# Optimization experiments

Hardware: AMD Instinct MI355X
Metric: run time of the kernel (lower is better)

Reference implementation:

```python
import jax, jax.numpy as jnp
import numpy as np

N_BRANCH, N_LAYER = 4, 3
B, T, D_IN = 4, 1024, 32
D_MODEL, D_INNER, D_STATE, D_CONV, DT_RANK = 128, 256, 16, 4, 8
EMBED = 64
MAX_NORM = 10.0  # safe_expmap0 tangent-norm clip
EPS = 1e-7


def setup_inputs() -> dict:
    key = jax.random.key(0)
    ks = jax.random.split(key, 12)
    def nrm(k, shp, s=0.02):
        return s * jax.random.normal(k, shp, dtype=jnp.float32)
    A_init = jnp.log(jnp.arange(1, D_STATE + 1, dtype=jnp.float32))
    return {
        "trend": jax.random.normal(ks[0], (B, T, D_IN), jnp.float32),
        "seasonal_coarse": jax.random.normal(ks[1], (B, T, D_IN), jnp.float32),
        "seasonal_fine": jax.random.normal(ks[2], (B, T, D_IN), jnp.float32),
        "residual": jax.random.normal(ks[3], (B, T, D_IN), jnp.float32),
        "W_ip": nrm(ks[4], (N_BRANCH, D_IN, D_MODEL)),
        "b_ip": jnp.zeros((N_BRANCH, D_MODEL), jnp.float32),
        "W_in": nrm(ks[5], (N_BRANCH, N_LAYER, D_MODEL, 2 * D_INNER)),
        "conv_w": nrm(ks[6], (N_BRANCH, N_LAYER, D_INNER, D_CONV), 0.1),
        "conv_b": jnp.zeros((N_BRANCH, N_LAYER, D_INNER), jnp.float32),
        "W_x": nrm(ks[7], (N_BRANCH, N_LAYER, D_INNER, DT_RANK + 2 * D_STATE)),
        "W_dt": nrm(ks[8], (N_BRANCH, N_LAYER, DT_RANK, D_INNER), 0.1),
        "b_dt": jnp.full((N_BRANCH, N_LAYER, D_INNER), -4.6, jnp.float32),  # softplus ~ 0.01
        "A_log": jnp.broadcast_to(A_init, (N_BRANCH, N_LAYER, D_INNER, D_STATE)),
        "D_param": jnp.ones((N_BRANCH, N_LAYER, D_INNER), jnp.float32),
        "W_out": nrm(ks[9], (N_BRANCH, N_LAYER, D_INNER, D_MODEL)),
        "W_op": nrm(ks[10], (N_BRANCH, D_MODEL, EMBED)),
        "b_op": jnp.zeros((N_BRANCH, EMBED), jnp.float32),
        "eff_scale": jnp.asarray(0.1, jnp.float32),
    }


def _mamba_layer(x, Win, cw, cb, Wx, Wdt, bdt, Alog, Dp, Wout):
    # x: [B, T, d_model]
    Tlen = x.shape[1]
    xz = x @ Win                                   # [B,T,2*di]
    xp, z = jnp.split(xz, 2, axis=-1)
    # causal depthwise conv1d, kernel D_CONV
    xpad = jnp.pad(xp, ((0, 0), (D_CONV - 1, 0), (0, 0)))
    xc = sum(xpad[:, k:k + Tlen, :] * cw[:, k] for k in range(D_CONV))
    xc = jax.nn.silu(xc + cb)                      # [B,T,di]
    dbl = xc @ Wx                                  # [B,T,r+2s]
    dt = jax.nn.softplus(dbl[..., :DT_RANK] @ Wdt + bdt)   # [B,T,di]
    Bm = dbl[..., DT_RANK:DT_RANK + D_STATE]       # [B,T,s]
    Cm = dbl[..., DT_RANK + D_STATE:]              # [B,T,s]
    A = -jnp.exp(Alog)                             # [di,s]
    dA = jnp.exp(dt[..., None] * A)                # [B,T,di,s]
    dBx = (dt * xc)[..., None] * Bm[:, :, None, :] # [B,T,di,s]

    def step(h, inp):
        dA_t, dBx_t, C_t = inp
        h = dA_t * h + dBx_t
        return h, jnp.einsum('bds,bs->bd', h, C_t)

    h0 = jnp.zeros((x.shape[0], D_INNER, D_STATE), x.dtype)
    _, ys = jax.lax.scan(step, h0, (jnp.swapaxes(dA, 0, 1),
                                     jnp.swapaxes(dBx, 0, 1),
                                     jnp.swapaxes(Cm, 0, 1)))
    y = jnp.swapaxes(ys, 0, 1) + Dp * xc
    return (y * jax.nn.silu(z)) @ Wout


def _embed(x, Wip, bip, Wins, cws, cbs, Wxs, Wdts, bdts, Alogs, Dps, Wouts, Wop, bop):
    h = x @ Wip + bip
    for l in range(N_LAYER):
        h = _mamba_layer(h, Wins[l], cws[l], cbs[l], Wxs[l], Wdts[l], bdts[l],
                         Alogs[l], Dps[l], Wouts[l])
    return h.mean(axis=1) @ Wop + bop              # [B, EMBED]


def _expmap0(v):
    # safe expmap0 on Lorentz (k=1): clip tangent norm at MAX_NORM
    n = jnp.linalg.norm(v, axis=-1, keepdims=True)
    nc = jnp.clip(n, EPS, MAX_NORM)
    v = v * (nc / jnp.maximum(n, EPS))
    return jnp.concatenate([jnp.cosh(nc), jnp.sinh(nc) / nc * v], axis=-1)


def _projx(x):
    sp = x[..., 1:]
    t = jnp.sqrt(1.0 + jnp.sum(sp * sp, axis=-1, keepdims=True))
    return jnp.concatenate([t, sp], axis=-1)


def _logmap0(x):
    sp = x[..., 1:]
    t = jnp.maximum(x[..., :1], 1.0 + EPS)
    d = jnp.arccosh(t)
    spn = jnp.maximum(jnp.linalg.norm(sp, axis=-1, keepdims=True), EPS)
    return d * sp / spn


def _forward(trend, seasonal_coarse, seasonal_fine, residual,
             W_ip, b_ip, W_in, conv_w, conv_b, W_x, W_dt, b_dt,
             A_log, D_param, W_out, W_op, b_op, eff_scale):
    xs = [trend, seasonal_coarse, seasonal_fine, residual]
    z_t = [
        _embed(xs[b], W_ip[b], b_ip[b], W_in[b], conv_w[b], conv_b[b], W_x[b],
               W_dt[b], b_dt[b], A_log[b], D_param[b], W_out[b], W_op[b], b_op[b])
        for b in range(N_BRANCH)
    ]
    es = jnp.tanh(eff_scale)
    z_h = [_projx(_expmap0(z * es)) for z in z_t]
    us = [_logmap0(zh) for zh in z_h]
    combined_tangent = us[0] + us[1] + us[2] + us[3]
    combined_h = _projx(_expmap0(combined_tangent * es))
    return (*z_t, *z_h, combined_tangent, combined_h)


def reference(trend, seasonal_coarse, seasonal_fine, residual,
              W_ip, b_ip, W_in, conv_w, conv_b, W_x, W_dt, b_dt,
              A_log, D_param, W_out, W_op, b_op, eff_scale):
    return _forward(trend, seasonal_coarse, seasonal_fine, residual,
                    W_ip, b_ip, W_in, conv_w, conv_b, W_x, W_dt, b_dt,
                    A_log, D_param, W_out, W_op, b_op, eff_scale)
```

## Files before the change

### kernel.cpp

```cpp
#include <hip/hip_runtime.h>
#include <math.h>

#define NBR 4
#define NLAY 3
#define Bk 4
#define Tk 1024
#define DIN 32
#define DMODEL 128
#define DINNER 256
#define DSTATE 16
#define DTRANK 8
#define EMBEDk 64
#define BT (Bk*Tk)
#define EPSF 1e-7f
#define MAXNF 10.0f
#define LCH 64
#define NCH (Tk/LCH)
#define UF 8
#define NWB 320

typedef __bf16 bf16x8 __attribute__((ext_vector_type(8)));
typedef float  f32x4  __attribute__((ext_vector_type(4)));
typedef unsigned short u16x8 __attribute__((ext_vector_type(8)));
typedef unsigned short u16x4 __attribute__((ext_vector_type(4)));

__device__ __forceinline__ float siluf(float x){ return x / (1.f + __expf(-x)); }
__device__ __forceinline__ float softplusf(float x){ return (x > 20.f) ? x : log1pf(__expf(x)); }
__device__ __forceinline__ unsigned short f2b(float x){
    union { float f; unsigned u; } v; v.f = x;
    unsigned r = v.u + 0x7FFF + ((v.u >> 16) & 1);
    return (unsigned short)(r >> 16);
}
__device__ __forceinline__ float b2f(unsigned short u){
    union { unsigned u; float f; } v; v.u = ((unsigned)u) << 16; return v.f;
}

__device__ __forceinline__ void gll16(const void* g, void* l){
    __builtin_amdgcn_global_load_lds(
        (const __attribute__((address_space(1))) unsigned int*)g,
        (__attribute__((address_space(3))) unsigned int*)l,
        16, 0, 0);
}

__device__ __forceinline__ void dA_pow8(float q, int sh, float* dA){
    const float q2 = q * q, q4 = q2 * q2, q8 = q4 * q4;
    const float f = sh ? q8 : 1.0f;
    dA[0] = q * f;       dA[1] = q2 * f;
    dA[2] = q2 * q * f;  dA[3] = q4 * f;
    dA[4] = q4 * q * f;  dA[5] = q4 * q2 * f;
    dA[6] = q4 * q2 * q * f; dA[7] = q8 * f;
}

template<int MODE>
__global__ __launch_bounds__(256) void bgemm_k(
    const unsigned short* __restrict__ Ab, long aBr, int K,
    const unsigned short* __restrict__ Bt, long bBr,
    unsigned short* __restrict__ Cu0, long cu0Br,
    unsigned short* __restrict__ Cu1, long cu1Br,
    float* __restrict__ Cf, long cfBr,
    const float* __restrict__ bias, long biasBr)
{
    const int br = blockIdx.z;
    Ab += (long)br * aBr;
    Bt += (long)br * bBr;
    Cu0 += (long)br * cu0Br;
    if (MODE == 0) Cu1 += (long)br * cu1Br;
    if (MODE == 3) { Cf += (long)br * cfBr; bias += (long)br * biasBr; }
    const int m0 = blockIdx.x * 64, n0 = blockIdx.y * 64;
    __shared__ __align__(16) unsigned short As[8 * 64 * 8];
    __shared__ __align__(16) unsigned short Bs[8 * 64 * 8];
    const int tid = threadIdx.x;
    const int lane = tid & 63, w = tid >> 6;
    const int wm = w >> 1, wn = w & 1;
    const int quad = lane >> 4, l15 = lane & 15;
    f32x4 acc00 = {0,0,0,0}, acc01 = {0,0,0,0}, acc10 = {0,0,0,0}, acc11 = {0,0,0,0};
    for (int kc = 0; kc < K; kc += 64) {
        #pragma unroll
        for (int it = 0; it < 2; ++it) {
            const int kch = w + it * 4;
            gll16(Ab + (long)(m0 + lane) * K + kc + kch * 8, &As[(kch * 64) * 8]);
            gll16(Bt + (long)(n0 + lane) * K + kc + kch * 8, &Bs[(kch * 64) * 8]);
        }
        __syncthreads();
        #pragma unroll
        for (int k0 = 0; k0 < 64; k0 += 32) {
            const int kch = (k0 >> 3) + quad;
            bf16x8 a0 = *(const bf16x8*)&As[(kch * 64 + wm * 32 +      l15) * 8];
            bf16x8 a1 = *(const bf16x8*)&As[(kch * 64 + wm * 32 + 16 + l15) * 8];
            bf16x8 b0 = *(const bf16x8*)&Bs[(kch * 64 + wn * 32 +      l15) * 8];
            bf16x8 b1 = *(const bf16x8*)&Bs[(kch * 64 + wn * 32 + 16 + l15) * 8];
            acc00 = __builtin_amdgcn_mfma_f32_16x16x32_bf16(a0, b0, acc00, 0, 0, 0);
            acc01 = __builtin_amdgcn_mfma_f32_16x16x32_bf16(a0, b1, acc01, 0, 0, 0);
            acc10 = __builtin_amdgcn_mfma_f32_16x16x32_bf16(a1, b0, acc10, 0, 0, 0);
            acc11 = __builtin_amdgcn_mfma_f32_16x16x32_bf16(a1, b1, acc11, 0, 0, 0);
        }
        __syncthreads();
    }
    #pragma unroll
    for (int e = 0; e < 4; ++e) {
        f32x4 a = (e == 0) ? acc00 : (e == 1) ? acc01 : (e == 2) ? acc10 : acc11;
        const int msub = (e >> 1) * 16, nsub = (e & 1) * 16;
        const int col = n0 + wn * 32 + nsub + l15;
        #pragma unroll
        for (int r = 0; r < 4; ++r) {
            const int row = m0 + wm * 32 + msub + quad * 4 + r;
            const float v = a[r];
            if (MODE == 0) {
                if (n0 < 256) Cu0[(long)row * 256 + col] = f2b(v);
                else          Cu1[(long)row * 256 + (col - 256)] = f2b(siluf(v));
            } else {
                if (col < 256)      Cu0[(long)row * 256 + col] = f2b(softplusf(v + bias[col]));
                else if (col < 288) Cf[(long)row * 32 + (col - 256)] = v;
            }
        }
    }
}

__global__ __launch_bounds__(256) void sgemmWT_k(
    const float* __restrict__ Wout, const float* __restrict__ Win,
    const float* __restrict__ Wip, const float* __restrict__ bip,
    const float* __restrict__ Wop,
    unsigned short* __restrict__ WfT, float* __restrict__ Weq,
    float* __restrict__ Wcomb)
{
    const int z = blockIdx.z;
    const int tid = threadIdx.x;
    const int tx = tid & 15, ty = tid >> 4;
    __shared__ float As_[32][68];
    __shared__ float Bs_[32][68];
    float acc[4][4] = {};
    if (z < 8) {
        const int p = z >> 2, br = z & 3;
        const float* A  = Wout + (long)(br * NLAY + p) * DINNER * DMODEL;
        const float* Bw = Win  + (long)(br * NLAY + p + 1) * DMODEL * 512;
        const int m0 = blockIdx.x * 64, n0 = blockIdx.y * 64;
        for (int kc = 0; kc < DMODEL; kc += 32) {
            #pragma unroll
            for (int it = 0; it < 2; ++it) {
                int id = tid + it * 256;
                int r = id >> 3, c4 = (id & 7) << 2;
                float4 v = *(const float4*)(A + (long)(m0 + r) * DMODEL + kc + c4);
                As_[c4+0][r] = v.x; As_[c4+1][r] = v.y; As_[c4+2][r] = v.z; As_[c4+3][r] = v.w;
                int rb = id >> 4, cb = (id & 15) << 2;
                *(float4*)&Bs_[rb][cb] = *(const float4*)(Bw + (long)(kc + rb) * 512 + n0 + cb);
            }
            __syncthreads();
            #pragma unroll
            for (int kk = 0; kk < 32; ++kk) {
                float4 a4 = *(const float4*)&As_[kk][ty << 2];
                float4 b4 = *(const float4*)&Bs_[kk][tx << 2];
                float av[4] = {a4.x, a4.y, a4.z, a4.w};
                float bv[4] = {b4.x, b4.y, b4.z, b4.w};
                #pragma unroll
                for (int i = 0; i < 4; ++i)
                    #pragma unroll
                    for (int j = 0; j < 4; ++j)
                        acc[i][j] = fmaf(av[i], bv[j], acc[i][j]);
            }
            __syncthreads();
        }
        unsigned short* o = WfT + (long)z * 512 * 256;
        const int row0 = m0 + (ty << 2), col = n0 + (tx << 2);
        #pragma unroll
        for (int j = 0; j < 4; ++j) {
            u16x4 v;
            #pragma unroll
            for (int i = 0; i < 4; ++i) v[i] = f2b(acc[i][j]);
            *(u16x4*)(o + (long)(col + j) * 256 + row0) = v;
        }
    } else if (z == 8) {
        const int br = blockIdx.x;
        const float* A  = Wip + (long)br * DIN * DMODEL;
        const float* bp = bip + (long)br * DMODEL;
        const float* Bw = Win + (long)br * NLAY * DMODEL * 512;
        const int n0 = blockIdx.y * 64;
        for (int kc = 0; kc < DMODEL; kc += 32) {
            #pragma unroll
            for (int it = 0; it < 2; ++it) {
                int id = tid + it * 256;
                int r = id >> 3, c4 = (id & 7) << 2;
                float4 v;
                if (r < 32)       v = *(const float4*)(A + (long)r * DMODEL + kc + c4);
                else if (r == 32) v = *(const float4*)(bp + kc + c4);
                else              { v.x = 0.f; v.y = 0.f; v.z = 0.f; v.w = 0.f; }
                As_[c4+0][r] = v.x; As_[c4+1][r] = v.y; As_[c4+2][r] = v.z; As_[c4+3][r] = v.w;
                int rb = id >> 4, cb = (id & 15) << 2;
                *(float4*)&Bs_[rb][cb] = *(const float4*)(Bw + (long)(kc + rb) * 512 + n0 + cb);
            }
            __syncthreads();
            #pragma unroll
            for (int kk = 0; kk < 32; ++kk) {
                float4 a4 = *(const float4*)&As_[kk][ty << 2];
                float4 b4 = *(const float4*)&Bs_[kk][tx << 2];
                float av[4] = {a4.x, a4.y, a4.z, a4.w};
                float bv[4] = {b4.x, b4.y, b4.z, b4.w};
                #pragma unroll
                for (int i = 0; i < 4; ++i)
                    #pragma unroll
                    for (int j = 0; j < 4; ++j)
                        acc[i][j] = fmaf(av[i], bv[j], acc[i][j]);
            }
            __syncthreads();
        }
        float* C = Weq + (long)br * 33 * 512;
        const int col = n0 + (tx << 2);
        #pragma unroll
        for (int i = 0; i < 4; ++i) {
            const int row = (ty << 2) + i;
            if (row < 33) {
                float4 v4; v4.x = acc[i][0]; v4.y = acc[i][1]; v4.z = acc[i][2]; v4.w = acc[i][3];
                *(float4*)(C + (long)row * 512 + col) = v4;
            }
        }
    } else {
        if (blockIdx.y >= 4) return;
        const int br = blockIdx.y;
        const float* A  = Wout + (long)(br * NLAY + 2) * DINNER * DMODEL;
        const float* Bw = Wop  + (long)br * DMODEL * EMBEDk;
        const int m0 = blockIdx.x * 64;
        for (int kc = 0; kc < DMODEL; kc += 32) {
            #pragma unroll
            for (int it = 0; it < 2; ++it) {
                int id = tid + it * 256;
                int r = id >> 3, c4 = (id & 7) << 2;
                float4 v = *(const float4*)(A + (long)(m0 + r) * DMODEL + kc + c4);
                As_[c4+0][r] = v.x; As_[c4+1][r] = v.y; As_[c4+2][r] = v.z; As_[c4+3][r] = v.w;
                int rb = id >> 4, cb = (id & 15) << 2;
                if (cb < 64)
                    *(float4*)&Bs_[rb][cb] = *(const float4*)(Bw + (long)(kc + rb) * EMBEDk + cb);
            }
            __syncthreads();
            #pragma unroll
            for (int kk = 0; kk < 32; ++kk) {
                float4 a4 = *(const float4*)&As_[kk][ty << 2];
                float4 b4 = *(const float4*)&Bs_[kk][tx << 2];
                float av[4] = {a4.x, a4.y, a4.z, a4.w};
                float bv[4] = {b4.x, b4.y, b4.z, b4.w};
                #pragma unroll
                for (int i = 0; i < 4; ++i)
                    #pragma unroll
                    for (int j = 0; j < 4; ++j)
                        acc[i][j] = fmaf(av[i], bv[j], acc[i][j]);
            }
            __syncthreads();
        }
        float* C = Wcomb + (long)br * DINNER * EMBEDk;
        const int col = tx << 2;
        #pragma unroll
        for (int i = 0; i < 4; ++i) {
            const int row = m0 + (ty << 2) + i;
            float4 v4; v4.x = acc[i][0]; v4.y = acc[i][1]; v4.z = acc[i][2]; v4.w = acc[i][3];
            *(float4*)(C + (long)row * EMBEDk + col) = v4;
        }
    }
}

__global__ __launch_bounds__(256) void prepC_k(
    const float* __restrict__ Wx, const float* __restrict__ Wdt,
    unsigned short* __restrict__ o)
{
    const int n = blockIdx.x, bl = blockIdx.y;
    const int k = threadIdx.x;
    const float* WxP = Wx + (long)bl * DINNER * 40;
    float v;
    if (n < 256) {
        const float* WdtP = Wdt + (long)bl * DTRANK * DINNER;
        float s = 0.f;
        #pragma unroll
        for (int r = 0; r < 8; ++r) s = fmaf(WxP[k * 40 + r], WdtP[r * DINNER + n], s);
        v = s;
    } else if (n < 288) {
        v = WxP[k * 40 + 8 + (n - 256)];
    } else {
        v = 0.f;
    }
    o[(long)bl * NWB * DINNER + (long)n * DINNER + k] = f2b(v);
}

__global__ __launch_bounds__(256) void xgemm0_k(
    const float* __restrict__ A0, const float* __restrict__ A1,
    const float* __restrict__ A2, const float* __restrict__ A3,
    const float* __restrict__ Weq,
    unsigned short* __restrict__ zb, unsigned short* __restrict__ xpb)
{
    const int br = blockIdx.z;
    const float* A = (br == 1) ? A1 : (br == 2) ? A2 : (br == 3) ? A3 : A0;
    const float* W = Weq + (long)br * 33 * 512;
    unsigned short* Cz = zb + (long)br * BT * DINNER;
    unsigned short* Cb = xpb + (long)br * BT * DINNER;
    const int m0 = blockIdx.x * 64, n0 = blockIdx.y * 64;
    __shared__ float As_[32][68];
    __shared__ float Bs_[32][68];
    const int tid = threadIdx.x;
    const int tx = tid & 15, ty = tid >> 4;
    float acc[4][4] = {};
    {
        #pragma unroll
        for (int it = 0; it < 2; ++it) {
            int id = tid + it * 256;
            int r = id >> 3, c4 = (id & 7) << 2;
            float4 v = *(const float4*)(A + (long)(m0 + r) * DIN + c4);
            As_[c4+0][r] = v.x; As_[c4+1][r] = v.y; As_[c4+2][r] = v.z; As_[c4+3][r] = v.w;
            int rb = id >> 4, cb = (id & 15) << 2;
            *(float4*)&Bs_[rb][cb] = *(const float4*)(W + (long)rb * 512 + n0 + cb);
        }
        __syncthreads();
        #pragma unroll
        for (int kk = 0; kk < 32; ++kk) {
            float4 a4 = *(const float4*)&As_[kk][ty << 2];
            float4 b4 = *(const float4*)&Bs_[kk][tx << 2];
            float av[4] = {a4.x, a4.y, a4.z, a4.w};
            float bv[4] = {b4.x, b4.y, b4.z, b4.w};
            #pragma unroll
            for (int i = 0; i < 4; ++i)
                #pragma unroll
                for (int j = 0; j < 4; ++j)
                    acc[i][j] = fmaf(av[i], bv[j], acc[i][j]);
        }
    }
    const int col = n0 + (tx << 2);
    float be[4];
    #pragma unroll
    for (int j = 0; j < 4; ++j) be[j] = W[32 * 512 + col + j];
    #pragma unroll
    for (int i = 0; i < 4; ++i) {
        const int row = m0 + (ty << 2) + i;
        #pragma unroll
        for (int j = 0; j < 4; ++j) {
            const float v = acc[i][j] + be[j];
            if (n0 < 256) Cb[(long)row * 256 + col + j] = f2b(v);
            else          Cz[(long)row * 256 + (col - 256 + j)] = f2b(siluf(v));
        }
    }
}

__global__ __launch_bounds__(256) void conv_k(
    const unsigned short* __restrict__ xp, const float* __restrict__ cw,
    const float* __restrict__ cb, unsigned short* __restrict__ xcb, int layer)
{
    const int br = blockIdx.y;
    const long base = (long)br * BT * DINNER;
    const long idx8 = ((long)blockIdx.x * 256 + threadIdx.x) * 8;
    const int d0 = (int)(idx8 & (DINNER - 1));
    const long row = idx8 >> 8;
    const int t = (int)(row & (Tk - 1));
    const float* cwp = cw + ((long)(br * NLAY + layer) * DINNER + d0) * 4;
    const float* cbp = cb + (long)(br * NLAY + layer) * DINNER + d0;
    u16x8 in[4];
    #pragma unroll
    for (int k = 0; k < 4; ++k) {
        const int tt = t + k - 3;
        if (tt >= 0) {
            in[k] = *(const u16x8*)(xp + base + idx8 + (long)(k - 3) * DINNER);
        } else {
            #pragma unroll
            for (int j = 0; j < 8; ++j) in[k][j] = 0;
        }
    }
    u16x8 o;
    #pragma unroll
    for (int j = 0; j < 8; ++j) {
        float acc = cbp[j];
        #pragma unroll
        for (int k = 0; k < 4; ++k)
            acc = fmaf(b2f(in[k][j]), cwp[j * 4 + k], acc);
        o[j] = f2b(siluf(acc));
    }
    *(u16x8*)(xcb + base + idx8) = o;
}

__global__ __launch_bounds__(512) void scan1_k(
    const unsigned short* __restrict__ dtb, const unsigned short* __restrict__ xcb,
    const float* __restrict__ bcb, const float* __restrict__ Alog,
    float* __restrict__ recbuf, int layer)
{
    const int c = blockIdx.x, b = blockIdx.y, br = blockIdx.z;
    const int tid = threadIdx.x;
    const int d = tid >> 1, sh = tid & 1, s0 = sh << 3;
    const float* Ap = Alog + ((long)(br * NLAY + layer) * DINNER + d) * DSTATE + s0;
    float Aa[8]; bool pw = true;
    #pragma unroll
    for (int k = 0; k < 8; ++k) {
        Aa[k] = -__expf(Ap[k]);
        pw = pw && (fabsf(Aa[k] + (float)(s0 + k + 1)) < 1e-3f);
    }
    const long rbase = (long)br * BT + (long)b * Tk + (long)c * LCH;
    const unsigned short* dtp = dtb + rbase * DINNER + d;
    const unsigned short* xcp = xcb + rbase * DINNER + d;
    __shared__ float bcs[LCH * 32];
    ((float4*)bcs)[tid] = ((const float4*)(bcb + rbase * 32))[tid];
    float dtc[UF], xcc[UF];
    #pragma unroll
    for (int u = 0; u < UF; ++u) {
        dtc[u] = b2f(dtp[(long)u * DINNER]);
        xcc[u] = b2f(xcp[(long)u * DINNER]);
    }
    __syncthreads();
    float h[8];
    #pragma unroll
    for (int k = 0; k < 8; ++k) h[k] = 0.f;
    float sumdt = 0.f;
    for (int base = 0; base < LCH; base += UF) {
        const int nb = (base + UF < LCH) ? base + UF : base;
        float dtn[UF], xcn[UF];
        #pragma unroll
        for (int u = 0; u < UF; ++u) {
            dtn[u] = b2f(dtp[(long)(nb + u) * DINNER]);
            xcn[u] = b2f(xcp[(long)(nb + u) * DINNER]);
        }
        #pragma unroll
        for (int u = 0; u < UF; ++u) {
            const int t = base + u;
            const float dtv = dtc[u];
            const float dtxc = dtv * xcc[u];
            sumdt += dtv;
            float dA[8];
            if (pw) dA_pow8(__expf(-dtv), sh, dA);
            else {
                #pragma unroll
                for (int k = 0; k < 8; ++k) dA[k] = __expf(dtv * Aa[k]);
            }
            const float* bcT = bcs + t * 32 + s0;
            #pragma unroll
            for (int k = 0; k < 8; ++k)
                h[k] = fmaf(dA[k], h[k], dtxc * bcT[k]);
        }
        #pragma unroll
        for (int u = 0; u < UF; ++u) { dtc[u] = dtn[u]; xcc[u] = xcn[u]; }
    }
    float* sb = recbuf + (((long)(br * 4 + b) * (NCH - 1) + c) * 17) * 256 + d;
    #pragma unroll
    for (int k = 0; k < 8; ++k) sb[(s0 + k) * 256] = h[k];
    if (!sh) sb[16 * 256] = sumdt;
}

__global__ __launch_bounds__(512) void scan3_k(
    const unsigned short* __restrict__ dtb, const unsigned short* __restrict__ xcb,
    const float* __restrict__ bcb, const unsigned short* __restrict__ zb,
    const float* __restrict__ Alog, const float* __restrict__ Dpar,
    const float* __restrict__ recbuf, unsigned short* __restrict__ yzb, int layer)
{
    const int c = blockIdx.x, b = blockIdx.y, br = blockIdx.z;
    const int tid = threadIdx.x;
    const int d = tid >> 1, sh = tid & 1, s0 = sh << 3;
    const float* Ap = Alog + ((long)(br * NLAY + layer) * DINNER + d) * DSTATE + s0;
    float Aa[8]; bool pw = true;
    #pragma unroll
    for (int k = 0; k < 8; ++k) {
        Aa[k] = -__expf(Ap[k]);
        pw = pw && (fabsf(Aa[k] + (float)(s0 + k + 1)) < 1e-3f);
    }
    float h[8];
    #pragma unroll
    for (int k = 0; k < 8; ++k) h[k] = 0.f;
    if (c > 0) {
        const float* recB = recbuf + ((long)(br * 4 + b) * (NCH - 1)) * 17 * 256 + d;
        float rh[8], rs;
        #pragma unroll
        for (int k = 0; k < 8; ++k) rh[k] = recB[(s0 + k) * 256];
        rs = recB[16 * 256];
        for (int cc = 0; cc < c; ++cc) {
            float nh[8], ns = 0.f;
            if (cc + 1 < c) {
                const float* r2 = recB + (long)(cc + 1) * 17 * 256;
                #pragma unroll
                for (int k = 0; k < 8; ++k) nh[k] = r2[(s0 + k) * 256];
                ns = r2[16 * 256];
            } else {
                #pragma unroll
                for (int k = 0; k < 8; ++k) nh[k] = 0.f;
            }
            float P[8];
            if (pw) dA_pow8(__expf(-rs), sh, P);
            else {
                #pragma unroll
                for (int k = 0; k < 8; ++k) P[k] = __expf(rs * Aa[k]);
            }
            #pragma unroll
            for (int k = 0; k < 8; ++k) h[k] = fmaf(h[k], P[k], rh[k]);
            #pragma unroll
            for (int k = 0; k < 8; ++k) rh[k] = nh[k];
            rs = ns;
        }
    }
    const float Dp = Dpar[(br * NLAY + layer) * DINNER + d];
    const long rbase = (long)br * BT + (long)b * Tk + (long)c * LCH;
    const unsigned short* dtp = dtb + rbase * DINNER + d;
    const unsigned short* xcp = xcb + rbase * DINNER + d;
    const unsigned short* zp  = zb  + rbase * DINNER + d;
    unsigned short* yp = yzb + rbase * DINNER + d;
    __shared__ float bcs[LCH * 32];
    ((float4*)bcs)[tid] = ((const float4*)(bcb + rbase * 32))[tid];
    float dtc[UF], xcc[UF], zc[UF];
    #pragma unroll
    for (int u = 0; u < UF; ++u) {
        dtc[u] = b2f(dtp[(long)u * DINNER]);
        xcc[u] = b2f(xcp[(long)u * DINNER]);
        zc[u]  = b2f(zp[(long)u * DINNER]);
    }
    __syncthreads();
    for (int base = 0; base < LCH; base += UF) {
        const int nb = (base + UF < LCH) ? base + UF : base;
        float dtn[UF], xcn[UF], zn[UF];
        #pragma unroll
        for (int u = 0; u < UF; ++u) {
            dtn[u] = b2f(dtp[(long)(nb + u) * DINNER]);
            xcn[u] = b2f(xcp[(long)(nb + u) * DINNER]);
            zn[u]  = b2f(zp[(long)(nb + u) * DINNER]);
        }
        #pragma unroll
        for (int u = 0; u < UF; ++u) {
            const int t = base + u;
            const float dtv = dtc[u], xcv = xcc[u];
            const float dtxc = dtv * xcv;
            float dA[8];
            if (pw) dA_pow8(__expf(-dtv), sh, dA);
            else {
                #pragma unroll
                for (int k = 0; k < 8; ++k) dA[k] = __expf(dtv * Aa[k]);
            }
            const float* bcT = bcs + t * 32 + s0;
            #pragma unroll
            for (int k = 0; k < 8; ++k)
                h[k] = fmaf(dA[k], h[k], dtxc * bcT[k]);
            float y0 = 0.f, y1 = 0.f;
            const float* cT = bcs + t * 32 + 16 + s0;
            #pragma unroll
            for (int k = 0; k < 8; k += 2) {
                y0 = fmaf(h[k+0], cT[k+0], y0);
                y1 = fmaf(h[k+1], cT[k+1], y1);
            }
            const float yp_ = y0 + y1;
            const float ytot = yp_ + __shfl_xor(yp_, 1);
            if (!sh) {
                const float y = ytot + Dp * xcv;
                yp[(long)t * DINNER] = f2b(y * zc[u]);
            }
        }
        #pragma unroll
        for (int u = 0; u < UF; ++u) { dtc[u] = dtn[u]; xcc[u] = xcn[u]; zc[u] = zn[u]; }
    }
}

__global__ __launch_bounds__(256) void csum1_k(
    const unsigned short* __restrict__ yz, float* __restrict__ part)
{
    const int ch = blockIdx.x, brb = blockIdx.y;
    const int br = brb >> 2, b = brb & 3;
    const long rbase = (long)br * BT + (long)b * Tk + (long)ch * 128;
    const int tid = threadIdx.x;
    const int cg = tid & 31;
    const int ro = tid >> 5;
    const unsigned short* p = yz + (rbase + ro) * DINNER + cg * 8;
    float acc[8] = {0,0,0,0,0,0,0,0};
    for (int it = 0; it < 16; ++it) {
        u16x8 v = *(const u16x8*)(p + (long)it * 8 * DINNER);
        #pragma unroll
        for (int j = 0; j < 8; ++j) acc[j] += b2f(v[j]);
    }
    __shared__ float sm[8][256];
    #pragma unroll
    for (int j = 0; j < 8; ++j) sm[ro][cg * 8 + j] = acc[j];
    __syncthreads();
    float s = 0.f;
    #pragma unroll
    for (int r = 0; r < 8; ++r) s += sm[r][tid];
    part[((long)brb * 8 + ch) * 256 + tid] = s;
}

__global__ __launch_bounds__(256) void csum2_k(
    const float* __restrict__ part, const float* __restrict__ Wcomb,
    const float* __restrict__ bop, float* __restrict__ outzt)
{
    const int brb = blockIdx.x, br = brb >> 2;
    const int tid = threadIdx.x;
    __shared__ float vm[256];
    __shared__ float red[4][64];
    float s = 0.f;
    #pragma unroll
    for (int ch = 0; ch < 8; ++ch) s += part[((long)brb * 8 + ch) * 256 + tid];
    vm[tid] = s * (1.0f / Tk);
    __syncthreads();
    const float* Wc = Wcomb + (long)br * DINNER * EMBEDk;
    const int col = tid & 63, seg = tid >> 6;
    float a = 0.f;
    #pragma unroll 8
    for (int k = seg * 64; k < seg * 64 + 64; ++k)
        a = fmaf(vm[k], Wc[(long)k * EMBEDk + col], a);
    red[seg][col] = a;
    __syncthreads();
    if (tid < 64)
        outzt[brb * EMBEDk + tid] =
            red[0][tid] + red[1][tid] + red[2][tid] + red[3][tid] + bop[br * EMBEDk + tid];
}

__global__ __launch_bounds__(64) void final_k(
    const float* __restrict__ zt, float* __restrict__ out, const float* __restrict__ eff)
{
    const float es = tanhf(eff[0]);
    __shared__ float us[NBR][Bk][EMBEDk];
    const int t = threadIdx.x;
    if (t < 16) {
        const int br = t >> 2, b = t & 3;
        const float* z = zt + br * (Bk * EMBEDk) + b * EMBEDk;
        float n2 = 0.f;
        for (int e = 0; e < EMBEDk; ++e) { float v = z[e] * es; n2 = fmaf(v, v, n2); }
        const float n  = sqrtf(n2);
        const float nc = fminf(fmaxf(n, EPSF), MAXNF);
        const float sc = nc / fmaxf(n, EPSF);
        const float sh = sinhf(nc) / nc;
        const float fac = es * sc * sh;
        float* zh = out + 1024 + br * (Bk * (EMBEDk + 1)) + b * (EMBEDk + 1);
        float sp2 = 0.f;
        for (int e = 0; e < EMBEDk; ++e) {
            float spv = z[e] * fac;
            sp2 = fmaf(spv, spv, sp2);
            zh[1 + e] = spv;
            us[br][b][e] = spv;
        }
        const float t0 = sqrtf(1.f + sp2);
        zh[0] = t0;
        const float dd  = acoshf(fmaxf(t0, 1.f + EPSF));
        const float spn = fmaxf(sqrtf(sp2), EPSF);
        const float rr  = dd / spn;
        for (int e = 0; e < EMBEDk; ++e) us[br][b][e] *= rr;
    }
    __syncthreads();
    if (t < 4) {
        const int b = t;
        float ct[EMBEDk];
        float* cto = out + 2064 + b * EMBEDk;
        for (int e = 0; e < EMBEDk; ++e) {
            float v = us[0][b][e] + us[1][b][e] + us[2][b][e] + us[3][b][e];
            ct[e] = v; cto[e] = v;
        }
        float n2 = 0.f;
        for (int e = 0; e < EMBEDk; ++e) { float v = ct[e] * es; n2 = fmaf(v, v, n2); }
        const float n  = sqrtf(n2);
        const float nc = fminf(fmaxf(n, EPSF), MAXNF);
        const float sc = nc / fmaxf(n, EPSF);
        const float sh = sinhf(nc) / nc;
        const float fac = es * sc * sh;
        float* ch = out + 2320 + b * (EMBEDk + 1);
        float sp2 = 0.f;
        for (int e = 0; e < EMBEDk; ++e) {
            float spv = ct[e] * fac;
            sp2 = fmaf(spv, spv, sp2);
            ch[1 + e] = spv;
        }
        ch[0] = sqrtf(1.f + sp2);
    }
}

extern "C" void kernel_launch(void* const* d_in, const int* in_sizes, int n_in,
                              void* d_out, int out_size, void* d_ws, size_t ws_size,
                              hipStream_t stream)
{
    const float* X0 = (const float*)d_in[0];
    const float* X1 = (const float*)d_in[1];
    const float* X2 = (const float*)d_in[2];
    const float* X3 = (const float*)d_in[3];
    const float* W_ip   = (const float*)d_in[4];
    const float* b_ip   = (const float*)d_in[5];
    const float* W_in   = (const float*)d_in[6];
    const float* conv_w = (const float*)d_in[7];
    const float* conv_b = (const float*)d_in[8];
    const float* W_x    = (const float*)d_in[9];
    const float* W_dt   = (const float*)d_in[10];
    const float* b_dt   = (const float*)d_in[11];
    const float* A_log  = (const float*)d_in[12];
    const float* D_par  = (const float*)d_in[13];
    const float* W_out  = (const float*)d_in[14];
    const float* W_op   = (const float*)d_in[15];
    const float* b_op   = (const float*)d_in[16];
    const float* eff    = (const float*)d_in[17];
    float* out = (float*)d_out;
    float* ws  = (float*)d_ws;

    float* buf_bc = ws;
    float* part   = buf_bc + (long)NBR * BT * 32;
    float* recbuf = part + 32768;
    float* Weq    = recbuf + (long)16 * (NCH - 1) * 17 * 256;
    float* Wcomb  = Weq + 4 * 33 * 512;
    unsigned short* xp_bf = (unsigned short*)(Wcomb + 4 * 256 * 64);
    unsigned short* xc_bf = xp_bf + (long)NBR * BT * DINNER;
    unsigned short* z_bf  = xc_bf + (long)NBR * BT * DINNER;
    unsigned short* dt_bf = z_bf  + (long)NBR * BT * DINNER;
    unsigned short* yz_bf = dt_bf + (long)NBR * BT * DINNER;
    unsigned short* WfT   = yz_bf + (long)NBR * BT * DINNER;
    unsigned short* WcT   = WfT   + (long)8 * 512 * DINNER;

    prepC_k<<<dim3(NWB, NBR * NLAY), 256, 0, stream>>>(W_x, W_dt, WcT);
    sgemmWT_k<<<dim3(4, 8, 10), 256, 0, stream>>>(
        W_out, W_in, W_ip, b_ip, W_op, WfT, Weq, Wcomb);

    xgemm0_k<<<dim3(BT / 64, 8, NBR), 256, 0, stream>>>(
        X0, X1, X2, X3, Weq, z_bf, xp_bf);

    for (int l = 0; l < NLAY; ++l) {
        if (l > 0) {
            bgemm_k<0><<<dim3(BT / 64, 8, NBR), 256, 0, stream>>>(
                yz_bf, (long)BT * DINNER, DINNER,
                WfT + (long)(l - 1) * 4 * 512 * DINNER, (long)512 * DINNER,
                xp_bf, (long)BT * DINNER,
                z_bf, (long)BT * DINNER,
                nullptr, 0, nullptr, 0);
        }
        conv_k<<<dim3((BT * DINNER) / (256 * 8), NBR), 256, 0, stream>>>(
            xp_bf, conv_w, conv_b, xc_bf, l);
        bgemm_k<3><<<dim3(BT / 64, NWB / 64, NBR), 256, 0, stream>>>(
            xc_bf, (long)BT * DINNER, DINNER,
            WcT + (long)l * NWB * DINNER, (long)NLAY * NWB * DINNER,
            dt_bf, (long)BT * DINNER,
            nullptr, 0,
            buf_bc, (long)BT * 32,
            b_dt + l * DINNER, (long)NLAY * DINNER);
        scan1_k<<<dim3(NCH - 1, Bk, NBR), 512, 0, stream>>>(
            dt_bf, xc_bf, buf_bc, A_log, recbuf, l);
        scan3_k<<<dim3(NCH, Bk, NBR), 512, 0, stream>>>(
            dt_bf, xc_bf, buf_bc, z_bf, A_log, D_par, recbuf, yz_bf, l);
    }

    csum1_k<<<dim3(8, 16), 256, 0, stream>>>(yz_bf, part);
    csum2_k<<<16, 256, 0, stream>>>(part, Wcomb, b_op, out);
    final_k<<<1, 64, 0, stream>>>(out, out, eff);
}
```

Before: 424.0 us.

## Fuse conv into x-projection GEMM, fold weight prep and column sum

The depthwise causal conv plus SiLU is now computed inside a new GEMM kernel. Each block stages a 64-row xp tile with a 3-row halo in LDS, convolves it into a swizzled A tile, and multiplies by the combined dt/B/C weights, with each block covering 192 output columns. The prepC weight-building kernel is folded into the existing sgemmWT launch as extra z-slices. On the last layer, scan3 accumulates the y*z column sums directly, so the separate csum1 pass over yz goes away. This cuts kernel launches and global round trips of xc and yz. In exchange, both column-half blocks recompute the conv, and LDS use per block is higher.

```diff
diff --git a/kernel.cpp b/kernel.cpp
--- a/kernel.cpp
+++ b/kernel.cpp
@@ -17,7 +17,7 @@
 #define LCH 64
 #define NCH (Tk/LCH)
 #define UF 8
-#define NWB 320
+#define NWB 384
 
 typedef __bf16 bf16x8 __attribute__((ext_vector_type(8)));
 typedef float  f32x4  __attribute__((ext_vector_type(4)));
@@ -56,16 +56,13 @@
     const unsigned short* __restrict__ Ab, long aBr, int K,
     const unsigned short* __restrict__ Bt, long bBr,
     unsigned short* __restrict__ Cu0, long cu0Br,
-    unsigned short* __restrict__ Cu1, long cu1Br,
-    float* __restrict__ Cf, long cfBr,
-    const float* __restrict__ bias, long biasBr)
+    unsigned short* __restrict__ Cu1, long cu1Br)
 {
     const int br = blockIdx.z;
     Ab += (long)br * aBr;
     Bt += (long)br * bBr;
     Cu0 += (long)br * cu0Br;
-    if (MODE == 0) Cu1 += (long)br * cu1Br;
-    if (MODE == 3) { Cf += (long)br * cfBr; bias += (long)br * biasBr; }
+    Cu1 += (long)br * cu1Br;
     const int m0 = blockIdx.x * 64, n0 = blockIdx.y * 64;
     __shared__ __align__(16) unsigned short As[8 * 64 * 8];
     __shared__ __align__(16) unsigned short Bs[8 * 64 * 8];
@@ -105,12 +102,132 @@
         for (int r = 0; r < 4; ++r) {
             const int row = m0 + wm * 32 + msub + quad * 4 + r;
             const float v = a[r];
-            if (MODE == 0) {
-                if (n0 < 256) Cu0[(long)row * 256 + col] = f2b(v);
-                else          Cu1[(long)row * 256 + (col - 256)] = f2b(siluf(v));
-            } else {
-                if (col < 256)      Cu0[(long)row * 256 + col] = f2b(softplusf(v + bias[col]));
-                else if (col < 288) Cf[(long)row * 32 + (col - 256)] = v;
+            if (n0 < 256) Cu0[(long)row * 256 + col] = f2b(v);
+            else          Cu1[(long)row * 256 + (col - 256)] = f2b(siluf(v));
+        }
+    }
+}
+
+__global__ __launch_bounds__(256) void convgemm_k(
+    const unsigned short* __restrict__ xp, const unsigned short* __restrict__ WcT,
+    const float* __restrict__ cw, const float* __restrict__ cbias,
+    const float* __restrict__ bdtA,
+    unsigned short* __restrict__ xcb, unsigned short* __restrict__ dtb,
+    float* __restrict__ bcb, int layer)
+{
+    const int br = blockIdx.z, yb = blockIdx.y;
+    const int bl = br * NLAY + layer;
+    const int m0 = blockIdx.x * 64;
+    const int nbase = yb * 192;
+    const int tid = threadIdx.x;
+    const int lane = tid & 63, w = tid >> 6;
+    __shared__ __align__(16) unsigned short As[32 * 64 * 8];
+    __shared__ __align__(16) unsigned short U[17408];
+    unsigned short* xps = U;
+    unsigned short* Bs  = U;
+    const unsigned short* xpB = xp + (long)br * BT * 256;
+
+    #pragma unroll
+    for (int it = 0; it < 8; ++it) {
+        const int ub = it * 256 + w * 64;
+        gll16(xpB + (long)(m0 - 3) * 256 + (long)(ub + lane) * 8, &xps[ub * 8]);
+    }
+    {
+        const int ub = 2048 + w * 64;
+        if (ub + lane < 2144)
+            gll16(xpB + (long)(m0 - 3) * 256 + (long)(ub + lane) * 8, &xps[ub * 8]);
+    }
+    __syncthreads();
+
+    {
+        const int g = tid & 31, r0 = tid >> 5;
+        const int d0 = g * 8;
+        const int tloc0 = m0 & (Tk - 1);
+        float wv[8][4], bv[8];
+        #pragma unroll
+        for (int j = 0; j < 8; ++j) {
+            const float4 w4 = *(const float4*)(cw + ((long)bl * DINNER + d0 + j) * 4);
+            wv[j][0] = w4.x; wv[j][1] = w4.y; wv[j][2] = w4.z; wv[j][3] = w4.w;
+            bv[j] = cbias[bl * DINNER + d0 + j];
+        }
+        unsigned short* xcG = xcb + (long)br * BT * 256;
+        #pragma unroll
+        for (int i = 0; i < 8; ++i) {
+            const int r = r0 + i * 8;
+            u16x8 in[4];
+            #pragma unroll
+            for (int k = 0; k < 4; ++k)
+                in[k] = *(const u16x8*)&xps[(r + k) * 256 + d0];
+            u16x8 o;
+            #pragma unroll
+            for (int j = 0; j < 8; ++j) {
+                float a = bv[j];
+                #pragma unroll
+                for (int k = 0; k < 4; ++k)
+                    if (tloc0 + r + k - 3 >= 0)
+                        a = fmaf(b2f(in[k][j]), wv[j][k], a);
+                o[j] = f2b(siluf(a));
+            }
+            *(u16x8*)&As[((g * 64) + (r ^ (g & 7))) * 8] = o;
+            if (yb == 0) *(u16x8*)(xcG + (long)(m0 + r) * 256 + d0) = o;
+        }
+    }
+    __syncthreads();
+
+    const int wm = w >> 1, wn = w & 1;
+    const int quad = lane >> 4, l15 = lane & 15;
+    f32x4 acc[3][4];
+    #pragma unroll
+    for (int nt = 0; nt < 3; ++nt)
+        #pragma unroll
+        for (int e = 0; e < 4; ++e) { f32x4 zz = {0,0,0,0}; acc[nt][e] = zz; }
+    const unsigned short* Bt = WcT + (long)bl * NWB * DINNER;
+    for (int kc = 0; kc < 4; ++kc) {
+        #pragma unroll
+        for (int it = 0; it < 6; ++it) {
+            const int ub = it * 256 + w * 64;
+            const int u = ub + lane;
+            const int kch = u / 192, nl = u % 192;
+            gll16(Bt + (long)(nbase + nl) * 256 + kc * 64 + kch * 8, &Bs[ub * 8]);
+        }
+        __syncthreads();
+        #pragma unroll
+        for (int k0 = 0; k0 < 2; ++k0) {
+            const int kchL = k0 * 4 + quad;
+            const int kchG = kc * 8 + kchL;
+            const int xr = kchL;
+            bf16x8 a0 = *(const bf16x8*)&As[(kchG * 64 + ((wm * 32 +      l15) ^ xr)) * 8];
+            bf16x8 a1 = *(const bf16x8*)&As[(kchG * 64 + ((wm * 32 + 16 + l15) ^ xr)) * 8];
+            #pragma unroll
+            for (int nt = 0; nt < 3; ++nt) {
+                bf16x8 b0 = *(const bf16x8*)&Bs[(kchL * 192 + nt * 64 + wn * 32 +      l15) * 8];
+                bf16x8 b1 = *(const bf16x8*)&Bs[(kchL * 192 + nt * 64 + wn * 32 + 16 + l15) * 8];
+                acc[nt][0] = __builtin_amdgcn_mfma_f32_16x16x32_bf16(a0, b0, acc[nt][0], 0, 0, 0);
+                acc[nt][1] = __builtin_amdgcn_mfma_f32_16x16x32_bf16(a0, b1, acc[nt][1], 0, 0, 0);
+                acc[nt][2] = __builtin_amdgcn_mfma_f32_16x16x32_bf16(a1, b0, acc[nt][2], 0, 0, 0);
+                acc[nt][3] = __builtin_amdgcn_mfma_f32_16x16x32_bf16(a1, b1, acc[nt][3], 0, 0, 0);
+            }
+        }
+        __syncthreads();
+    }
+    {
+        const float* bdt = bdtA + (long)bl * DINNER;
+        unsigned short* dtO = dtb + (long)br * BT * 256;
+        float* bcO = bcb + (long)br * BT * 32;
+        #pragma unroll
+        for (int nt = 0; nt < 3; ++nt) {
+            #pragma unroll
+            for (int e = 0; e < 4; ++e) {
+                const f32x4 a = acc[nt][e];
+                const int msub = (e >> 1) * 16, nsub = (e & 1) * 16;
+                const int col = nbase + nt * 64 + wn * 32 + nsub + l15;
+                #pragma unroll
+                for (int r = 0; r < 4; ++r) {
+                    const int row = m0 + wm * 32 + msub + quad * 4 + r;
+                    const float v = a[r];
+                    if (col < 256)      dtO[(long)row * 256 + col] = f2b(softplusf(v + bdt[col]));
+                    else if (col < 288) bcO[(long)row * 32 + (col - 256)] = v;
+                }
             }
         }
     }
@@ -120,8 +237,9 @@
     const float* __restrict__ Wout, const float* __restrict__ Win,
     const float* __restrict__ Wip, const float* __restrict__ bip,
     const float* __restrict__ Wop,
+    const float* __restrict__ Wx, const float* __restrict__ Wdt,
     unsigned short* __restrict__ WfT, float* __restrict__ Weq,
-    float* __restrict__ Wcomb)
+    float* __restrict__ Wcomb, unsigned short* __restrict__ WcT)
 {
     const int z = blockIdx.z;
     const int tid = threadIdx.x;
@@ -212,7 +330,7 @@
                 *(float4*)(C + (long)row * 512 + col) = v4;
             }
         }
-    } else {
+    } else if (z == 9) {
         if (blockIdx.y >= 4) return;
         const int br = blockIdx.y;
         const float* A  = Wout + (long)(br * NLAY + 2) * DINNER * DMODEL;
@@ -252,29 +370,29 @@
             float4 v4; v4.x = acc[i][0]; v4.y = acc[i][1]; v4.z = acc[i][2]; v4.w = acc[i][3];
             *(float4*)(C + (long)row * EMBEDk + col) = v4;
         }
-    }
-}
-
-__global__ __launch_bounds__(256) void prepC_k(
-    const float* __restrict__ Wx, const float* __restrict__ Wdt,
-    unsigned short* __restrict__ o)
-{
-    const int n = blockIdx.x, bl = blockIdx.y;
-    const int k = threadIdx.x;
-    const float* WxP = Wx + (long)bl * DINNER * 40;
-    float v;
-    if (n < 256) {
+    } else {
+        const int bl = z - 10;
+        const int base = (blockIdx.x * 8 + blockIdx.y) * 12;
+        const float* WxP = Wx + (long)bl * DINNER * 40;
         const float* WdtP = Wdt + (long)bl * DTRANK * DINNER;
-        float s = 0.f;
-        #pragma unroll
-        for (int r = 0; r < 8; ++r) s = fmaf(WxP[k * 40 + r], WdtP[r * DINNER + n], s);
-        v = s;
-    } else if (n < 288) {
-        v = WxP[k * 40 + 8 + (n - 256)];
-    } else {
-        v = 0.f;
-    }
-    o[(long)bl * NWB * DINNER + (long)n * DINNER + k] = f2b(v);
+        unsigned short* o = WcT + (long)bl * NWB * DINNER;
+        #pragma unroll
+        for (int i = 0; i < 12; ++i) {
+            const int n = base + i;
+            float v;
+            if (n < 256) {
+                float s = 0.f;
+                #pragma unroll
+                for (int r = 0; r < 8; ++r) s = fmaf(WxP[tid * 40 + r], WdtP[r * DINNER + n], s);
+                v = s;
+            } else if (n < 288) {
+                v = WxP[tid * 40 + 8 + (n - 256)];
+            } else {
+                v = 0.f;
+            }
+            o[(long)n * DINNER + tid] = f2b(v);
+        }
+    }
 }
 
 __global__ __launch_bounds__(256) void xgemm0_k(
@@ -334,41 +452,6 @@
     }
 }
 
-__global__ __launch_bounds__(256) void conv_k(
-    const unsigned short* __restrict__ xp, const float* __restrict__ cw,
-    const float* __restrict__ cb, unsigned short* __restrict__ xcb, int layer)
-{
-    const int br = blockIdx.y;
-    const long base = (long)br * BT * DINNER;
-    const long idx8 = ((long)blockIdx.x * 256 + threadIdx.x) * 8;
-    const int d0 = (int)(idx8 & (DINNER - 1));
-    const long row = idx8 >> 8;
-    const int t = (int)(row & (Tk - 1));
-    const float* cwp = cw + ((long)(br * NLAY + layer) * DINNER + d0) * 4;
-    const float* cbp = cb + (long)(br * NLAY + layer) * DINNER + d0;
-    u16x8 in[4];
-    #pragma unroll
-    for (int k = 0; k < 4; ++k) {
-        const int tt = t + k - 3;
-        if (tt >= 0) {
-            in[k] = *(const u16x8*)(xp + base + idx8 + (long)(k - 3) * DINNER);
-        } else {
-            #pragma unroll
-            for (int j = 0; j < 8; ++j) in[k][j] = 0;
-        }
-    }
-    u16x8 o;
-    #pragma unroll
-    for (int j = 0; j < 8; ++j) {
-        float acc = cbp[j];
-        #pragma unroll
-        for (int k = 0; k < 4; ++k)
-            acc = fmaf(b2f(in[k][j]), cwp[j * 4 + k], acc);
-        o[j] = f2b(siluf(acc));
-    }
-    *(u16x8*)(xcb + base + idx8) = o;
-}
-
 __global__ __launch_bounds__(512) void scan1_k(
     const unsigned short* __restrict__ dtb, const unsigned short* __restrict__ xcb,
     const float* __restrict__ bcb, const float* __restrict__ Alog,
@@ -434,11 +517,13 @@
     if (!sh) sb[16 * 256] = sumdt;
 }
 
+template<int LAST>
 __global__ __launch_bounds__(512) void scan3_k(
     const unsigned short* __restrict__ dtb, const unsigned short* __restrict__ xcb,
     const float* __restrict__ bcb, const unsigned short* __restrict__ zb,
     const float* __restrict__ Alog, const float* __restrict__ Dpar,
-    const float* __restrict__ recbuf, unsigned short* __restrict__ yzb, int layer)
+    const float* __restrict__ recbuf, unsigned short* __restrict__ yzb,
+    float* __restrict__ part, int layer)
 {
     const int c = blockIdx.x, b = blockIdx.y, br = blockIdx.z;
     const int tid = threadIdx.x;
@@ -499,6 +584,7 @@
         zc[u]  = b2f(zp[(long)u * DINNER]);
     }
     __syncthreads();
+    float ysum = 0.f;
     for (int base = 0; base < LCH; base += UF) {
         const int nb = (base + UF < LCH) ? base + UF : base;
         float dtn[UF], xcn[UF], zn[UF];
@@ -532,40 +618,18 @@
             }
             const float yp_ = y0 + y1;
             const float ytot = yp_ + __shfl_xor(yp_, 1);
-            if (!sh) {
-                const float y = ytot + Dp * xcv;
+            const float y = ytot + Dp * xcv;
+            if (LAST) {
+                ysum += y * zc[u];
+            } else if (!sh) {
                 yp[(long)t * DINNER] = f2b(y * zc[u]);
             }
         }
         #pragma unroll
         for (int u = 0; u < UF; ++u) { dtc[u] = dtn[u]; xcc[u] = xcn[u]; zc[u] = zn[u]; }
     }
-}
-
-__global__ __launch_bounds__(256) void csum1_k(
-    const unsigned short* __restrict__ yz, float* __restrict__ part)
-{
-    const int ch = blockIdx.x, brb = blockIdx.y;
-    const int br = brb >> 2, b = brb & 3;
-    const long rbase = (long)br * BT + (long)b * Tk + (long)ch * 128;
-    const int tid = threadIdx.x;
-    const int cg = tid & 31;
-    const int ro = tid >> 5;
-    const unsigned short* p = yz + (rbase + ro) * DINNER + cg * 8;
-    float acc[8] = {0,0,0,0,0,0,0,0};
-    for (int it = 0; it < 16; ++it) {
-        u16x8 v = *(const u16x8*)(p + (long)it * 8 * DINNER);
-        #pragma unroll
-        for (int j = 0; j < 8; ++j) acc[j] += b2f(v[j]);
-    }
-    __shared__ float sm[8][256];
-    #pragma unroll
-    for (int j = 0; j < 8; ++j) sm[ro][cg * 8 + j] = acc[j];
-    __syncthreads();
-    float s = 0.f;
-    #pragma unroll
-    for (int r = 0; r < 8; ++r) s += sm[r][tid];
-    part[((long)brb * 8 + ch) * 256 + tid] = s;
+    if (LAST && !sh)
+        part[((long)(br * 4 + b) * 16 + c) * 256 + d] = ysum;
 }
 
 __global__ __launch_bounds__(256) void csum2_k(
@@ -578,7 +642,7 @@
     __shared__ float red[4][64];
     float s = 0.f;
     #pragma unroll
-    for (int ch = 0; ch < 8; ++ch) s += part[((long)brb * 8 + ch) * 256 + tid];
+    for (int ch = 0; ch < 16; ++ch) s += part[((long)brb * 16 + ch) * 256 + tid];
     vm[tid] = s * (1.0f / Tk);
     __syncthreads();
     const float* Wc = Wcomb + (long)br * DINNER * EMBEDk;
@@ -679,7 +743,7 @@
 
     float* buf_bc = ws;
     float* part   = buf_bc + (long)NBR * BT * 32;
-    float* recbuf = part + 32768;
+    float* recbuf = part + 65536;
     float* Weq    = recbuf + (long)16 * (NCH - 1) * 17 * 256;
     float* Wcomb  = Weq + 4 * 33 * 512;
     unsigned short* xp_bf = (unsigned short*)(Wcomb + 4 * 256 * 64);
@@ -690,9 +754,8 @@
     unsigned short* WfT   = yz_bf + (long)NBR * BT * DINNER;
     unsigned short* WcT   = WfT   + (long)8 * 512 * DINNER;
 
-    prepC_k<<<dim3(NWB, NBR * NLAY), 256, 0, stream>>>(W_x, W_dt, WcT);
-    sgemmWT_k<<<dim3(4, 8, 10), 256, 0, stream>>>(
-        W_out, W_in, W_ip, b_ip, W_op, WfT, Weq, Wcomb);
+    sgemmWT_k<<<dim3(4, 8, 22), 256, 0, stream>>>(
+        W_out, W_in, W_ip, b_ip, W_op, W_x, W_dt, WfT, Weq, Wcomb, WcT);
 
     xgemm0_k<<<dim3(BT / 64, 8, NBR), 256, 0, stream>>>(
         X0, X1, X2, X3, Weq, z_bf, xp_bf);
@@ -703,25 +766,22 @@
                 yz_bf, (long)BT * DINNER, DINNER,
                 WfT + (long)(l - 1) * 4 * 512 * DINNER, (long)512 * DINNER,
                 xp_bf, (long)BT * DINNER,
-                z_bf, (long)BT * DINNER,
-                nullptr, 0, nullptr, 0);
-        }
-        conv_k<<<dim3((BT * DINNER) / (256 * 8), NBR), 256, 0, stream>>>(
-            xp_bf, conv_w, conv_b, xc_bf, l);
-        bgemm_k<3><<<dim3(BT / 64, NWB / 64, NBR), 256, 0, stream>>>(
-            xc_bf, (long)BT * DINNER, DINNER,
-            WcT + (long)l * NWB * DINNER, (long)NLAY * NWB * DINNER,
-            dt_bf, (long)BT * DINNER,
-            nullptr, 0,
-            buf_bc, (long)BT * 32,
-            b_dt + l * DINNER, (long)NLAY * DINNER);
+                z_bf, (long)BT * DINNER);
+        }
+        convgemm_k<<<dim3(BT / 64, 2, NBR), 256, 0, stream>>>(
+            xp_bf, WcT + (long)l * NWB * DINNER * 0 + 0,
+            conv_w, conv_b, b_dt, xc_bf, dt_bf, buf_bc, l);
         scan1_k<<<dim3(NCH - 1, Bk, NBR), 512, 0, stream>>>(
             dt_bf, xc_bf, buf_bc, A_log, recbuf, l);
-        scan3_k<<<dim3(NCH, Bk, NBR), 512, 0, stream>>>(
-            dt_bf, xc_bf, buf_bc, z_bf, A_log, D_par, recbuf, yz_bf, l);
-    }
-
-    csum1_k<<<dim3(8, 16), 256, 0, stream>>>(yz_bf, part);
+        if (l < NLAY - 1) {
+            scan3_k<0><<<dim3(NCH, Bk, NBR), 512, 0, stream>>>(
+                dt_bf, xc_bf, buf_bc, z_bf, A_log, D_par, recbuf, yz_bf, nullptr, l);
+        } else {
+            scan3_k<1><<<dim3(NCH, Bk, NBR), 512, 0, stream>>>(
+                dt_bf, xc_bf, buf_bc, z_bf, A_log, D_par, recbuf, yz_bf, part, l);
+        }
+    }
+
     csum2_k<<<16, 256, 0, stream>>>(part, Wcomb, b_op, out);
     final_k<<<1, 64, 0, stream>>>(out, out, eff);
 }
```

Result: no change. 427.7 us (+0.9%).
